# Performance work log

Hardware: AMD Instinct MI355X
Metric: run time of the kernel (lower is better)

## Reference

```python
import jax, jax.numpy as jnp
import numpy as np

S, B, I, H, O = 512, 256, 64, 512, 25

def setup_inputs() -> dict:
    key = jax.random.key(0)
    ks = jax.random.split(key, 7)
    k = 1.0 / np.sqrt(H)  # torch nn.RNN / nn.Linear default init bound
    x = jax.random.normal(ks[0], (S, B, I), dtype=jnp.float32)
    W_ih = jax.random.uniform(ks[1], (H, I), jnp.float32, -k, k)
    W_hh = jax.random.uniform(ks[2], (H, H), jnp.float32, -k, k)
    b_ih = jax.random.uniform(ks[3], (H,), jnp.float32, -k, k)
    b_hh = jax.random.uniform(ks[4], (H,), jnp.float32, -k, k)
    W2 = jax.random.uniform(ks[5], (O, H), jnp.float32, -k, k)
    b2 = jax.random.uniform(ks[6], (O,), jnp.float32, -k, k)
    return {"x": x, "W_ih": W_ih, "W_hh": W_hh, "b_ih": b_ih, "b_hh": b_hh, "W2": W2, "b2": b2}

def reference(x, W_ih, W_hh, b_ih, b_hh, W2, b2):
    # Precompute input projection for all timesteps in one big GEMM: (S,B,H)
    xi = jnp.einsum('sbi,hi->sbh', x, W_ih) + b_ih
    h0 = jnp.zeros((x.shape[1], W_hh.shape[0]), dtype=x.dtype)
    W_hh_T = W_hh.T
    def step(h_prev, xi_t):
        h = jax.nn.relu(xi_t + h_prev @ W_hh_T + b_hh)
        return h, h
    _, out = jax.lax.scan(step, h0, xi)  # out: (S, B, H)
    # Faithful to original: out[:, -1, :] selects last batch element -> (S, H)
    y = out[:, -1, :] @ W2.T + b2  # (S, 25)
    return y
```

## Files before the change

### kernel.cpp

```cpp
#include <hip/hip_runtime.h>


#define S_ 512
#define B_ 256
#define I_ 64
#define H_ 512
#define O_ 25
#define G_ 16
#define R_ 32
#define T_ 512

__global__ __launch_bounds__(256) void rnn_pre(
    const float* __restrict__ x, const float* __restrict__ W_ih,
    const float* __restrict__ b_ih, const float* __restrict__ b_hh,
    float* __restrict__ xi, unsigned* __restrict__ mbox) {
  const int t = blockIdx.x;
  const int tid = threadIdx.x;
  const int o = blockIdx.y * 256 + tid;
  if (t == 0 && blockIdx.y == 0) {
    for (int j = tid; j < 2 * H_; j += 256) mbox[j] = 0x80000000u;
  }
  __shared__ float xr[I_];
  if (tid < I_) xr[tid] = x[(t * B_ + (B_ - 1)) * I_ + tid];
  __syncthreads();
  float acc = b_ih[o] + b_hh[o];
  const float4* wp = (const float4*)(W_ih + o * I_);
#pragma unroll
  for (int j = 0; j < I_ / 4; ++j) {
    float4 w4 = wp[j];
    acc += w4.x * xr[4 * j] + w4.y * xr[4 * j + 1] + w4.z * xr[4 * j + 2] +
           w4.w * xr[4 * j + 3];
  }
  xi[t * H_ + o] = acc;
}

__global__ __launch_bounds__(T_) void rnn_seq(
    const float* __restrict__ W_hh, const float* __restrict__ xi,
    float* __restrict__ hseq, unsigned* __restrict__ mbox) {
  const int tid = threadIdx.x;
  const int b = blockIdx.x;
  const int lane = tid & 63;
  const int wv = tid >> 6;
  const int seg = lane & 15;
  const int row_l = wv * 4 + (lane >> 4);
  const int row = b * R_ + row_l;
  const int own_lo = b * R_;
  const bool fin = (seg == 0);

  __shared__ float h_l[2][H_];

  float w[32];
  {
    const float4* wrow = (const float4*)(W_hh + row * H_);
#pragma unroll
    for (int j = 0; j < 8; ++j) {
      float4 v = wrow[seg + 16 * j];
      w[4 * j] = v.x; w[4 * j + 1] = v.y; w[4 * j + 2] = v.z; w[4 * j + 3] = v.w;
    }
  }
  for (int n = tid; n < H_; n += T_) h_l[0][n] = 0.0f;

  float xiv = fin ? xi[row] : 0.0f;
  __syncthreads();

  const int e = (tid < H_ - R_) ? (tid + ((tid >= own_lo) ? R_ : 0)) : -1;

  for (int s = 0; s < S_; ++s) {
    const float* hr = h_l[s & 1];
    float* hw = h_l[(s + 1) & 1];
    const unsigned phase = (unsigned)((s >> 1) & 1);
    unsigned* const buf = mbox + (s & 1) * H_;

    float a0 = 0.f, a1 = 0.f, a2 = 0.f, a3 = 0.f;
    const float4* hp = (const float4*)hr;
#pragma unroll
    for (int j = 0; j < 8; ++j) {
      float4 hv = hp[seg + 16 * j];
      a0 = fmaf(w[4 * j + 0], hv.x, a0);
      a1 = fmaf(w[4 * j + 1], hv.y, a1);
      a2 = fmaf(w[4 * j + 2], hv.z, a2);
      a3 = fmaf(w[4 * j + 3], hv.w, a3);
    }
    float acc = (a0 + a1) + (a2 + a3);
    acc += __shfl_xor(acc, 1, 64);
    acc += __shfl_xor(acc, 2, 64);
    acc += __shfl_xor(acc, 4, 64);
    acc += __shfl_xor(acc, 8, 64);

    if (fin) {
      float sum = acc + xiv;
      float h = (sum > 0.0f) ? sum : 0.0f;
      hw[row] = h;
      hseq[s * H_ + row] = h;
      __hip_atomic_store(&buf[row], __float_as_uint(h) | (phase << 31),
                         __ATOMIC_RELAXED, __HIP_MEMORY_SCOPE_AGENT);
    }

    if (s == S_ - 1) break;

    if (fin) xiv = xi[(s + 1) * H_ + row];

    if (e >= 0) {
      unsigned p;
      do {
        p = __hip_atomic_load(&buf[e], __ATOMIC_RELAXED, __HIP_MEMORY_SCOPE_AGENT);
      } while ((p >> 31) != phase);
      hw[e] = __uint_as_float(p & 0x7fffffffu);
    }
    __syncthreads();
  }
}

__global__ __launch_bounds__(256) void rnn_post(
    const float* __restrict__ hseq, const float* __restrict__ W2,
    const float* __restrict__ b2, float* __restrict__ y) {
  const int t = blockIdx.x;
  const int tid = threadIdx.x;
  __shared__ float hl[H_];
  __shared__ float part[256];
  for (int n = tid; n < H_; n += 256) hl[n] = hseq[t * H_ + n];
  __syncthreads();
  const int o = tid >> 3;
  const int seg = tid & 7;
  float acc = 0.0f;
  if (o < O_) {
    const float4* wp = (const float4*)(W2 + o * H_ + seg * 64);
    const float4* hp = (const float4*)(hl + seg * 64);
#pragma unroll
    for (int j = 0; j < 16; ++j) {
      float4 w4 = wp[j];
      float4 h4 = hp[j];
      acc += w4.x * h4.x + w4.y * h4.y + w4.z * h4.z + w4.w * h4.w;
    }
  }
  part[tid] = acc;
  __syncthreads();
  if (tid < O_) {
    float sum = 0.0f;
#pragma unroll
    for (int j = 0; j < 8; ++j) sum += part[tid * 8 + j];
    y[t * O_ + tid] = sum + b2[tid];
  }
}

extern "C" void kernel_launch(void* const* d_in, const int* in_sizes, int n_in,
                              void* d_out, int out_size, void* d_ws, size_t ws_size,
                              hipStream_t stream) {
  const float* x    = (const float*)d_in[0];
  const float* W_ih = (const float*)d_in[1];
  const float* W_hh = (const float*)d_in[2];
  const float* b_ih = (const float*)d_in[3];
  const float* b_hh = (const float*)d_in[4];
  const float* W2   = (const float*)d_in[5];
  const float* b2   = (const float*)d_in[6];
  float* y = (float*)d_out;

  float* xi   = (float*)d_ws;
  float* hseq = xi + S_ * H_;
  unsigned* mbox = (unsigned*)(hseq + S_ * H_);

  rnn_pre<<<dim3(S_, 2), 256, 0, stream>>>(x, W_ih, b_ih, b_hh, xi, mbox);
  rnn_seq<<<G_, T_, 0, stream>>>(W_hh, xi, hseq, mbox);
  rnn_post<<<S_, 256, 0, stream>>>(hseq, W2, b2, y);
}
```

Before: 819.6 us.

## Confine recurrent blocks to one XCC and exchange hidden state through local L2

Launches 256 blocks and elects eight that share one XCC (read from the hardware register) to run the recurrence; the rest exit. Each elected block owns 64 hidden rows. Per-step hidden values go out as 64-bit step-tagged words to an L2-local mailbox read with sc0 loads, and are also written to an agent-scope fallback mailbox that is polled every eighth try. Keeping cross-block exchange within one XCC's L2 is meant to cut per-step synchronisation latency. The cost is fewer blocks doing the math, more registers per thread, and reliance on inline asm cache-scope behaviour.

```diff
diff --git a/kernel.cpp b/kernel.cpp
--- a/kernel.cpp
+++ b/kernel.cpp
@@ -6,19 +6,27 @@
 #define I_ 64
 #define H_ 512
 #define O_ 25
-#define G_ 16
-#define R_ 32
-#define T_ 512
+#define W_ 8
+#define RW_ 64
+#define TW_ 512
+#define NB_ 256
+
+typedef unsigned long long u64;
 
 __global__ __launch_bounds__(256) void rnn_pre(
     const float* __restrict__ x, const float* __restrict__ W_ih,
     const float* __restrict__ b_ih, const float* __restrict__ b_hh,
-    float* __restrict__ xi, unsigned* __restrict__ mbox) {
+    float* __restrict__ xi, u64* __restrict__ l2box,
+    u64* __restrict__ l3box, unsigned* __restrict__ elect) {
   const int t = blockIdx.x;
   const int tid = threadIdx.x;
   const int o = blockIdx.y * 256 + tid;
   if (t == 0 && blockIdx.y == 0) {
-    for (int j = tid; j < 2 * H_; j += 256) mbox[j] = 0x80000000u;
+    for (int j = tid; j < 2 * H_; j += 256) {
+      l2box[j] = 0ull;
+      l3box[j] = 0ull;
+    }
+    if (tid < 9) elect[tid] = 0u;
   }
   __shared__ float xr[I_];
   if (tid < I_) xr[tid] = x[(t * B_ + (B_ - 1)) * I_ + tid];
@@ -34,48 +42,68 @@
   xi[t * H_ + o] = acc;
 }
 
-__global__ __launch_bounds__(T_) void rnn_seq(
+__global__ __launch_bounds__(TW_) void rnn_seq(
     const float* __restrict__ W_hh, const float* __restrict__ xi,
-    float* __restrict__ hseq, unsigned* __restrict__ mbox) {
+    float* __restrict__ hseq, u64* __restrict__ l2box,
+    u64* __restrict__ l3box, unsigned* __restrict__ elect) {
   const int tid = threadIdx.x;
-  const int b = blockIdx.x;
-  const int lane = tid & 63;
-  const int wv = tid >> 6;
-  const int seg = lane & 15;
-  const int row_l = wv * 4 + (lane >> 4);
-  const int row = b * R_ + row_l;
-  const int own_lo = b * R_;
+
+  __shared__ int role_s;
+  if (tid == 0) {
+    unsigned xcc;
+    asm volatile("s_getreg_b32 %0, hwreg(HW_REG_XCC_ID)" : "=s"(xcc));
+    xcc &= 7u;
+    unsigned tk = atomicAdd(&elect[xcc], 1u);
+    int role = -1;
+    if (tk < W_) {
+      if (tk == W_ - 1) atomicCAS(&elect[8], 0u, xcc + 1u);
+      unsigned win;
+      do {
+        win = __hip_atomic_load(&elect[8], __ATOMIC_RELAXED,
+                                __HIP_MEMORY_SCOPE_AGENT);
+      } while (win == 0u);
+      if (win == xcc + 1u) role = (int)tk;
+    }
+    role_s = role;
+  }
+  __syncthreads();
+  const int b = role_s;
+  if (b < 0) return;
+
+  const int seg = tid & 7;
+  const int row_l = tid >> 3;
+  const int row = b * RW_ + row_l;
+  const int own_lo = b * RW_;
   const bool fin = (seg == 0);
 
   __shared__ float h_l[2][H_];
 
-  float w[32];
+  float w[64];
   {
     const float4* wrow = (const float4*)(W_hh + row * H_);
 #pragma unroll
-    for (int j = 0; j < 8; ++j) {
-      float4 v = wrow[seg + 16 * j];
+    for (int j = 0; j < 16; ++j) {
+      float4 v = wrow[seg + 8 * j];
       w[4 * j] = v.x; w[4 * j + 1] = v.y; w[4 * j + 2] = v.z; w[4 * j + 3] = v.w;
     }
   }
-  for (int n = tid; n < H_; n += T_) h_l[0][n] = 0.0f;
-
+  for (int n = tid; n < H_; n += TW_) h_l[0][n] = 0.0f;
   float xiv = fin ? xi[row] : 0.0f;
   __syncthreads();
 
-  const int e = (tid < H_ - R_) ? (tid + ((tid >= own_lo) ? R_ : 0)) : -1;
+  const int e = (tid < H_ - RW_) ? (tid + ((tid >= own_lo) ? RW_ : 0)) : -1;
 
   for (int s = 0; s < S_; ++s) {
     const float* hr = h_l[s & 1];
     float* hw = h_l[(s + 1) & 1];
-    const unsigned phase = (unsigned)((s >> 1) & 1);
-    unsigned* const buf = mbox + (s & 1) * H_;
+    const unsigned want = (unsigned)(s + 1);
+    const int boff = (s & 1) * H_;
 
     float a0 = 0.f, a1 = 0.f, a2 = 0.f, a3 = 0.f;
     const float4* hp = (const float4*)hr;
 #pragma unroll
-    for (int j = 0; j < 8; ++j) {
-      float4 hv = hp[seg + 16 * j];
+    for (int j = 0; j < 16; ++j) {
+      float4 hv = hp[seg + 8 * j];
       a0 = fmaf(w[4 * j + 0], hv.x, a0);
       a1 = fmaf(w[4 * j + 1], hv.y, a1);
       a2 = fmaf(w[4 * j + 2], hv.z, a2);
@@ -85,27 +113,36 @@
     acc += __shfl_xor(acc, 1, 64);
     acc += __shfl_xor(acc, 2, 64);
     acc += __shfl_xor(acc, 4, 64);
-    acc += __shfl_xor(acc, 8, 64);
 
     if (fin) {
-      float sum = acc + xiv;
-      float h = (sum > 0.0f) ? sum : 0.0f;
+      float h = fmaxf(acc + xiv, 0.0f);
       hw[row] = h;
       hseq[s * H_ + row] = h;
-      __hip_atomic_store(&buf[row], __float_as_uint(h) | (phase << 31),
-                         __ATOMIC_RELAXED, __HIP_MEMORY_SCOPE_AGENT);
+      u64 pk = ((u64)want << 32) | (u64)__float_as_uint(h);
+      asm volatile("global_store_dwordx2 %0, %1, off"
+                   :: "v"(l2box + boff + row), "v"(pk) : "memory");
+      __hip_atomic_store(&l3box[boff + row], pk, __ATOMIC_RELAXED,
+                         __HIP_MEMORY_SCOPE_AGENT);
     }
 
     if (s == S_ - 1) break;
-
     if (fin) xiv = xi[(s + 1) * H_ + row];
 
     if (e >= 0) {
-      unsigned p;
-      do {
-        p = __hip_atomic_load(&buf[e], __ATOMIC_RELAXED, __HIP_MEMORY_SCOPE_AGENT);
-      } while ((p >> 31) != phase);
-      hw[e] = __uint_as_float(p & 0x7fffffffu);
+      const u64* ap = l2box + boff + e;
+      u64 q;
+      int it = 0;
+      while (true) {
+        asm volatile("global_load_dwordx2 %0, %1, off sc0\n\ts_waitcnt vmcnt(0)"
+                     : "=v"(q) : "v"(ap) : "memory");
+        if ((unsigned)(q >> 32) == want) break;
+        if ((++it & 7) == 0) {
+          q = __hip_atomic_load(&l3box[boff + e], __ATOMIC_RELAXED,
+                                __HIP_MEMORY_SCOPE_AGENT);
+          if ((unsigned)(q >> 32) == want) break;
+        }
+      }
+      hw[e] = __uint_as_float((unsigned)q);
     }
     __syncthreads();
   }
@@ -157,9 +194,12 @@
 
   float* xi   = (float*)d_ws;
   float* hseq = xi + S_ * H_;
-  unsigned* mbox = (unsigned*)(hseq + S_ * H_);
-
-  rnn_pre<<<dim3(S_, 2), 256, 0, stream>>>(x, W_ih, b_ih, b_hh, xi, mbox);
-  rnn_seq<<<G_, T_, 0, stream>>>(W_hh, xi, hseq, mbox);
+  u64* l2box  = (u64*)(hseq + S_ * H_);
+  u64* l3box  = l2box + 2 * H_;
+  unsigned* elect = (unsigned*)(l3box + 2 * H_);
+
+  rnn_pre<<<dim3(S_, 2), 256, 0, stream>>>(x, W_ih, b_ih, b_hh, xi,
+                                           l2box, l3box, elect);
+  rnn_seq<<<NB_, TW_, 0, stream>>>(W_hh, xi, hseq, l2box, l3box, elect);
   rnn_post<<<S_, 256, 0, stream>>>(hseq, W2, b2, y);
 }
```

New measurement: 1.288 ms. 1.57x slower.
